# Optimization experiments

Hardware: AMD Instinct MI355X
Metric: run time of the kernel (lower is better)

## Reference

```python
import jax, jax.numpy as jnp
from jax import lax
import numpy as np


def _conv2d(x, w, b, pad):
    # x: NCHW, w: OIHW
    o = lax.conv_general_dilated(x, w, window_strides=(1, 1),
                                 padding=[(pad, pad), (pad, pad)],
                                 dimension_numbers=('NCHW', 'OIHW', 'NCHW'))
    return o + b[None, :, None, None]


def _maxpool(x, kh, kw):
    return lax.reduce_window(x, -jnp.inf, lax.max,
                             window_dimensions=(1, 1, kh, kw),
                             window_strides=(1, 1, kh, kw),
                             padding='VALID')


def _l2norm(x, axis):
    n = jnp.sqrt(jnp.sum(x * x, axis=axis, keepdims=True))
    return x / jnp.maximum(n, 1e-12)


def setup_inputs() -> dict:
    key = jax.random.key(0)
    ks = jax.random.split(key, 12)
    d = {}
    d['x'] = jax.random.normal(ks[0], (16, 128, 40, 200), dtype=jnp.float32)
    d['cluster_centers'] = jax.random.uniform(ks[1], (64, 128), dtype=jnp.float32)
    d['conv_w'] = jax.random.normal(ks[2], (64, 128, 1, 1), dtype=jnp.float32) * 0.05
    d['conv_b'] = jax.random.normal(ks[3], (64,), dtype=jnp.float32) * 0.05
    d['w1'] = jax.random.normal(ks[4], (256, 128, 5, 5), dtype=jnp.float32) * 0.02
    d['b1'] = jax.random.normal(ks[5], (256,), dtype=jnp.float32) * 0.02
    d['w2'] = jax.random.normal(ks[6], (512, 256, 5, 5), dtype=jnp.float32) * 0.02
    d['b2'] = jax.random.normal(ks[7], (512,), dtype=jnp.float32) * 0.02
    d['w3'] = jax.random.normal(ks[8], (1024, 512, 5, 5), dtype=jnp.float32) * 0.02
    d['b3'] = jax.random.normal(ks[9], (1024,), dtype=jnp.float32) * 0.02
    d['mlp_w'] = jax.random.normal(ks[10], (256, 9216), dtype=jnp.float32) * 0.01
    d['mlp_b'] = jax.random.normal(ks[11], (256,), dtype=jnp.float32) * 0.01
    return d


def reference(x, cluster_centers, conv_w, conv_b, w1, b1, w2, b2, w3, b3, mlp_w, mlp_b):
    N, C, H, W = x.shape
    K = conv_w.shape[0]
    P = H * W

    # soft assignment: 1x1 conv -> softmax over cluster axis
    sa = _conv2d(x, conv_w, conv_b, 0).reshape(N, K, P)
    a = jax.nn.softmax(sa, axis=1)                      # [N, K, P]

    x_flat = x.reshape(N, C, P)
    # sum_p a[n,k,p] * (x[n,c,p] - centers[k,c])  -- algebraically equal to
    # the explicit NxKxCxP residual tensor, computed without materializing it.
    vlad = jnp.einsum('nkp,ncp->nkc', a, x_flat) \
           - a.sum(axis=-1)[:, :, None] * cluster_centers[None, :, :]
    vlad = _l2norm(vlad, axis=2)                        # intra-norm per cluster
    vlad = _l2norm(vlad.reshape(N, K * C), axis=1)      # [N, K*C]

    # CNN branch
    h = _conv2d(x, w1, b1, 2)
    h = jnp.where(h >= 0, h, 0.2 * h)                   # LeakyReLU(0.2)
    h = _maxpool(h, 2, 2)
    h = _conv2d(h, w2, b2, 2)
    h = jnp.where(h >= 0, h, 0.2 * h)
    h = _maxpool(h, 4, 4)
    h = _conv2d(h, w3, b3, 2)
    h = _maxpool(h, 5, 25)                              # -> [N, 1024, 1, 1]
    x_feat = _l2norm(h.reshape(N, -1), axis=1)          # [N, 1024]

    feat = jnp.concatenate([vlad, x_feat], axis=1)      # [N, 9216]
    out = feat @ mlp_w.T + mlp_b
    return _l2norm(out, axis=1)
```

## Files before the change

kernel.cpp:

```cpp
#include <hip/hip_runtime.h>
#include <math.h>

#define K_ 64
#define C_ 128
#define NB 16
#define P_ 8000

typedef float f32x4 __attribute__((ext_vector_type(4)));
typedef short s16x8 __attribute__((ext_vector_type(8)));

__device__ __forceinline__ short f2bf(float v) {
    unsigned u = __float_as_uint(v);
    u += 0x7FFFu + ((u >> 16) & 1u);
    return (short)(u >> 16);
}
__device__ __forceinline__ float bf2f(ushort u) { return __uint_as_float(((unsigned)u) << 16); }

__device__ __forceinline__ void stage16(const void* g, void* l) {
    __builtin_amdgcn_global_load_lds(
        (const __attribute__((address_space(1))) void*)g,
        (__attribute__((address_space(3))) void*)l, 16, 0, 0);
}

__global__ void k_transpose_tiled(const float* __restrict__ in, float* __restrict__ out,
                                  int Co, int E)
{
    __shared__ float t[32][33];
    const int e0  = blockIdx.x * 32;
    const int co0 = blockIdx.y * 32;
    for (int i = threadIdx.y; i < 32; i += 8) {
        int co = co0 + i, e = e0 + threadIdx.x;
        t[i][threadIdx.x] = (co < Co && e < E) ? in[(size_t)co * E + e] : 0.f;
    }
    __syncthreads();
    for (int i = threadIdx.y; i < 32; i += 8) {
        int e = e0 + i, co = co0 + threadIdx.x;
        if (e < E && co < Co) out[(size_t)e * Co + co] = t[threadIdx.x][i];
    }
}

__global__ void k_nchw_to_nhwc(const float* __restrict__ in, ushort* __restrict__ out,
                               int C, int P)
{
    __shared__ ushort t[32][33];
    const int n  = blockIdx.z;
    const int p0 = blockIdx.x * 32;
    const int c0 = blockIdx.y * 32;
    for (int i = threadIdx.y; i < 32; i += 8) {
        int c = c0 + i, p = p0 + threadIdx.x;
        t[i][threadIdx.x] = (c < C && p < P) ? (ushort)f2bf(in[((size_t)n * C + c) * P + p]) : 0;
    }
    __syncthreads();
    for (int i = threadIdx.y; i < 32; i += 8) {
        int p = p0 + i, c = c0 + threadIdx.x;
        if (p < P && c < C) out[((size_t)n * P + p) * C + c] = t[threadIdx.x][i];
    }
}

__global__ void k_wprep(const float* __restrict__ w, short* __restrict__ wb,
                        int Co, int Cin, int total)
{
    int idx = blockIdx.x * blockDim.x + threadIdx.x;
    if (idx >= total) return;
    int cl = idx & 31;
    int rest = idx >> 5;
    int co = rest % Co;
    int rest2 = rest / Co;
    int t = rest2 % 25;
    int ck = rest2 / 25;
    float v = w[((size_t)co * Cin + (ck << 5) + cl) * 25 + t];
    wb[idx] = f2bf(v);
}

template<int SR, int NC, int WR, int WC16, int IS3, int PL>
__global__ __launch_bounds__(256) void k_conv_mfma(
    const ushort* __restrict__ in, const s16x8* __restrict__ wb,
    const float* __restrict__ bias, ushort* __restrict__ outb, float* __restrict__ outf,
    const ushort* __restrict__ zg,
    int Cin, int Co, int H, int W, int WT, int leaky, int nck, int xpc, int PT)
{
    constexpr int NT   = 8;
    constexpr int TOT  = SR * NC * 4;
    constexpr int TOTP = (TOT + 63) & ~63;
    __shared__ s16x8 xin[TOTP];

    const int tid  = threadIdx.x;
    const int lane = tid & 63;
    const int wid  = tid >> 6;
    const int wm   = wid;
    const int n16  = lane & 15;
    const int g    = lane >> 4;

    const int lid  = blockIdx.x;
    const int xcd  = lid & 7;
    const int rrr  = lid >> 3;
    const int co_blk = xcd / xpc;
    const int posn = rrr * xpc + (xcd % xpc);
    const int n    = posn / PT;
    const int bx   = posn % PT;

    const int h0  = IS3 ? 0 : (bx / WT) * WR;
    const int w0  = IS3 ? 0 : (bx % WT) * (WC16 * 16);
    const int ks  = IS3 ? bx : 0;
    const int co0 = co_blk * 256;

    int ph[NT], pw[NT];
    if (IS3) {
        #pragma unroll
        for (int nt = 0; nt < NT; ++nt) {
            int pos = nt * 16 + n16;
            int h = pos / 25;
            int w = pos - h * 25;
            if (h > 4) { h = 0; w = 0; }
            ph[nt] = h; pw[nt] = w;
        }
    }

    f32x4 acc[4][NT];
    #pragma unroll
    for (int i = 0; i < 4; ++i)
        #pragma unroll
        for (int j = 0; j < NT; ++j) acc[i][j] = f32x4{0.f, 0.f, 0.f, 0.f};

    const int ck0 = IS3 ? ks * nck : 0;
    const int ckend = ck0 + nck;

    auto stage_input = [&](int ck) {
        for (int c = wid; c * 64 < TOTP; c += 4) {
            int u = c * 64 + lane;
            int row = u / (NC * 4);
            int rem = u - row * (NC * 4);
            int col = rem >> 2;
            int s   = rem & 3;
            int g8  = (s - (col >> 1) - row) & 3;
            int gh = h0 + row - 2, gw = w0 + col - 2;
            const void* src =
                (u < TOT && (unsigned)gh < (unsigned)H && (unsigned)gw < (unsigned)W)
                ? (const void*)(in + ((size_t)(n * H + gh) * W + gw) * Cin + (ck << 5) + (g8 << 3))
                : (const void*)zg;
            stage16(src, (void*)&xin[c * 64]);
        }
    };

    for (int ck = ck0; ck < ckend; ++ck) {
        if (ck != ck0) __syncthreads();
        stage_input(ck);
        __syncthreads();

        const s16x8* wbc = wb + ((size_t)(ck * 25) * Co + co0 + wm * 64 + n16) * 4 + g;

        s16x8 wreg[3][4];
        #pragma unroll
        for (int mt = 0; mt < 4; ++mt) wreg[0][mt] = wbc[mt * 64];
        #pragma unroll
        for (int mt = 0; mt < 4; ++mt) wreg[1][mt] = wbc[(size_t)Co * 4 + mt * 64];

        #pragma unroll
        for (int t = 0; t < 25; ++t) {
            if (t < 23) {
                const s16x8* wn = wbc + (size_t)(t + 2) * Co * 4;
                #pragma unroll
                for (int mt = 0; mt < 4; ++mt) wreg[(t + 2) % 3][mt] = wn[mt * 64];
            }
            const int r = t / 5, s = t - (t / 5) * 5;

            s16x8 bf[NT];
            #pragma unroll
            for (int nt = 0; nt < NT; ++nt) {
                int row, col;
                if (IS3) { row = ph[nt] + r; col = pw[nt] + s; }
                else {
                    int rr = nt / WC16, cc = nt - rr * WC16;
                    row = rr + r;
                    col = cc * 16 + n16 + s;
                }
                bf[nt] = xin[(row * NC + col) * 4 + ((g + (col >> 1) + row) & 3)];
            }
            __builtin_amdgcn_s_setprio(1);
            #pragma unroll
            for (int mt = 0; mt < 4; ++mt)
                #pragma unroll
                for (int nt = 0; nt < NT; ++nt)
                    acc[mt][nt] = __builtin_amdgcn_mfma_f32_16x16x32_bf16(
                        wreg[t % 3][mt], bf[nt], acc[mt][nt], 0, 0, 0);
            __builtin_amdgcn_s_setprio(0);
        }
    }

    if constexpr (IS3) {
        #pragma unroll
        for (int mt = 0; mt < 4; ++mt) {
            #pragma unroll
            for (int reg = 0; reg < 4; ++reg) {
                const int co = co0 + wm * 64 + mt * 16 + g * 4 + reg;
                #pragma unroll
                for (int nt = 0; nt < NT; ++nt) {
                    int pos = nt * 16 + n16;
                    if (pos < 125)
                        outf[((size_t)(ks * NB + n) * Co + co) * 125 + pos] = acc[mt][nt][reg];
                }
            }
        }
    } else if constexpr (PL == 2) {
        const int Hout = H >> 1, Wout = W >> 1;
        #pragma unroll
        for (int mt = 0; mt < 4; ++mt) {
            const int cb = co0 + wm * 64 + mt * 16 + g * 4;
            #pragma unroll
            for (int pr = 0; pr < 2; ++pr) {
                #pragma unroll
                for (int cc = 0; cc < 2; ++cc) {
                    ushort4 pkd;
                    #pragma unroll
                    for (int reg = 0; reg < 4; ++reg) {
                        float a0 = acc[mt][(2 * pr) * 2 + cc][reg] + bias[cb + reg];
                        float a1 = acc[mt][(2 * pr + 1) * 2 + cc][reg] + bias[cb + reg];
                        a0 = (a0 >= 0.f) ? a0 : 0.2f * a0;
                        a1 = (a1 >= 0.f) ? a1 : 0.2f * a1;
                        float m = fmaxf(a0, a1);
                        m = fmaxf(m, __shfl_xor(m, 1));
                        ((ushort*)&pkd)[reg] = (ushort)f2bf(m);
                    }
                    if ((n16 & 1) == 0) {
                        int ho = (h0 >> 1) + pr;
                        int wo = (w0 >> 1) + cc * 8 + (n16 >> 1);
                        if (wo < Wout)
                            *(ushort4*)(outb + ((size_t)(n * Hout + ho) * Wout + wo) * Co + cb) = pkd;
                    }
                }
            }
        }
    } else if constexpr (PL == 4) {
        const int Hout = H >> 2, Wout = W >> 2;
        #pragma unroll
        for (int mt = 0; mt < 4; ++mt) {
            const int cb = co0 + wm * 64 + mt * 16 + g * 4;
            #pragma unroll
            for (int cc = 0; cc < 2; ++cc) {
                ushort4 pkd;
                #pragma unroll
                for (int reg = 0; reg < 4; ++reg) {
                    float m = -INFINITY;
                    #pragma unroll
                    for (int rr = 0; rr < 4; ++rr) {
                        float a = acc[mt][rr * 2 + cc][reg] + bias[cb + reg];
                        a = (a >= 0.f) ? a : 0.2f * a;
                        m = fmaxf(m, a);
                    }
                    m = fmaxf(m, __shfl_xor(m, 1));
                    m = fmaxf(m, __shfl_xor(m, 2));
                    ((ushort*)&pkd)[reg] = (ushort)f2bf(m);
                }
                if ((n16 & 3) == 0) {
                    int ho = h0 >> 2;
                    int wo = (w0 >> 2) + cc * 4 + (n16 >> 2);
                    if (wo < Wout)
                        *(ushort4*)(outb + ((size_t)(n * Hout + ho) * Wout + wo) * Co + cb) = pkd;
                }
            }
        }
    } else {
        #pragma unroll
        for (int mt = 0; mt < 4; ++mt) {
            const int cobase = co0 + wm * 64 + mt * 16 + g * 4;
            const float b0 = bias[cobase + 0];
            const float b1 = bias[cobase + 1];
            const float b2 = bias[cobase + 2];
            const float b3 = bias[cobase + 3];
            #pragma unroll
            for (int nt = 0; nt < NT; ++nt) {
                int rr = nt / WC16, cc = nt - rr * WC16;
                int h  = h0 + rr;
                int wp = w0 + cc * 16 + n16;
                if (h < H && wp < W) {
                    float v0 = acc[mt][nt][0] + b0;
                    float v1 = acc[mt][nt][1] + b1;
                    float v2 = acc[mt][nt][2] + b2;
                    float v3 = acc[mt][nt][3] + b3;
                    if (leaky) {
                        v0 = (v0 >= 0.f) ? v0 : 0.2f * v0;
                        v1 = (v1 >= 0.f) ? v1 : 0.2f * v1;
                        v2 = (v2 >= 0.f) ? v2 : 0.2f * v2;
                        v3 = (v3 >= 0.f) ? v3 : 0.2f * v3;
                    }
                    ushort4 pkd;
                    pkd.x = (ushort)f2bf(v0);
                    pkd.y = (ushort)f2bf(v1);
                    pkd.z = (ushort)f2bf(v2);
                    pkd.w = (ushort)f2bf(v3);
                    *(ushort4*)(outb + ((size_t)(n * H + h) * W + wp) * Co + cobase) = pkd;
                }
            }
        }
    }
}

__global__ __launch_bounds__(256) void k_vlad_partial(
    const float* __restrict__ x,
    const float* __restrict__ convw_t,
    const float* __restrict__ convb,
    float* __restrict__ pv,
    float* __restrict__ pa)
{
    __shared__ float xs[C_][64];
    __shared__ float als[64][K_];
    __shared__ float pgsum[4][K_];

    const int tid = threadIdx.x;
    const int chunk = blockIdx.x;
    const int n = blockIdx.y;
    const int p0 = chunk * 64;

    const float* xn = x + (size_t)n * C_ * P_ + p0;
    for (int i = tid; i < C_ * 64; i += 256) {
        int c = i >> 6, pp = i & 63;
        xs[c][pp] = xn[(size_t)c * P_ + pp];
    }
    __syncthreads();

    const int k  = tid & 63;
    const int pg = tid >> 6;

    float sa[16];
    const float bk = convb[k];
    #pragma unroll
    for (int j = 0; j < 16; ++j) sa[j] = bk;
    for (int c = 0; c < C_; ++c) {
        float wv = convw_t[c * K_ + k];
        const float4* xp = (const float4*)&xs[c][pg * 16];
        #pragma unroll
        for (int q = 0; q < 4; ++q) {
            float4 xv = xp[q];
            sa[q*4+0] += wv * xv.x;
            sa[q*4+1] += wv * xv.y;
            sa[q*4+2] += wv * xv.z;
            sa[q*4+3] += wv * xv.w;
        }
    }

    float asum_loc = 0.f;
    #pragma unroll
    for (int j = 0; j < 16; ++j) {
        float m = sa[j];
        for (int d = 32; d >= 1; d >>= 1) m = fmaxf(m, __shfl_xor(m, d));
        float e = __expf(sa[j] - m);
        float s = e;
        for (int d = 32; d >= 1; d >>= 1) s += __shfl_xor(s, d);
        float a = e / s;
        als[pg * 16 + j][k] = a;
        asum_loc += a;
    }
    pgsum[pg][k] = asum_loc;
    __syncthreads();
    if (tid < K_) {
        pa[((size_t)n * 125 + chunk) * K_ + tid] =
            pgsum[0][tid] + pgsum[1][tid] + pgsum[2][tid] + pgsum[3][tid];
    }

    const int q = pg;
    float acc[32];
    #pragma unroll
    for (int j = 0; j < 32; ++j) acc[j] = 0.f;
    for (int p = 0; p < 64; p += 4) {
        float a0 = als[p+0][k], a1 = als[p+1][k], a2 = als[p+2][k], a3 = als[p+3][k];
        #pragma unroll
        for (int j = 0; j < 32; ++j) {
            const float4 xv = *(const float4*)&xs[q*32 + j][p];
            acc[j] += a0*xv.x + a1*xv.y + a2*xv.z + a3*xv.w;
        }
    }
    float* pvp = pv + ((((size_t)n * 125 + chunk) * K_ + k) * C_ + q * 32);
    #pragma unroll
    for (int j = 0; j < 32; ++j) pvp[j] = acc[j];
}

__global__ void k_vlad_reduce(const float* __restrict__ pv, float* __restrict__ vlad_raw)
{
    int idx = blockIdx.x * blockDim.x + threadIdx.x;
    if (idx >= NB * 8192) return;
    int n = idx >> 13;
    int rest = idx & 8191;
    const float* p = pv + (size_t)n * 125 * 8192 + rest;
    float s = 0.f;
    for (int ch = 0; ch < 125; ++ch) s += p[(size_t)ch * 8192];
    vlad_raw[(size_t)n * 8192 + rest] = s;
}

__global__ void k_asum_reduce(const float* __restrict__ pa, float* __restrict__ asum)
{
    int idx = blockIdx.x * blockDim.x + threadIdx.x;
    if (idx >= NB * K_) return;
    const float* p = pa + (size_t)(idx >> 6) * 125 * K_ + (idx & 63);
    float s = 0.f;
    for (int ch = 0; ch < 125; ++ch) s += p[ch * K_];
    asum[idx] = s;
}

__global__ __launch_bounds__(128) void k_vlad_finalize(
    const float* __restrict__ vlad_raw, const float* __restrict__ asum,
    const float* __restrict__ centers, float* __restrict__ feat)
{
    __shared__ float red[2];
    const int k = blockIdx.x, n = blockIdx.y, c = threadIdx.x;
    float v = vlad_raw[((size_t)n * K_ + k) * C_ + c] - asum[n * K_ + k] * centers[k * C_ + c];
    float ss = v * v;
    for (int d = 32; d >= 1; d >>= 1) ss += __shfl_xor(ss, d);
    if ((threadIdx.x & 63) == 0) red[threadIdx.x >> 6] = ss;
    __syncthreads();
    float denom = fmaxf(sqrtf(red[0] + red[1]), 1e-12f);
    feat[(size_t)n * 9216 + k * C_ + c] = v / denom;
}

__global__ void k_pool3_feat(const float* __restrict__ part, const float* __restrict__ bias,
                             float* __restrict__ feat)
{
    int idx = blockIdx.x * blockDim.x + threadIdx.x;
    if (idx >= NB * 1024) return;
    int n = idx >> 10, c = idx & 1023;
    const size_t kstride = (size_t)NB * 1024 * 125;
    const float* p = part + ((size_t)n * 1024 + c) * 125;
    const float b = bias[c];
    float m = -INFINITY;
    for (int i = 0; i < 125; ++i) {
        float s = 0.f;
        #pragma unroll
        for (int ksl = 0; ksl < 8; ++ksl) s += p[i + ksl * kstride];
        m = fmaxf(m, b + s);
    }
    feat[(size_t)n * 9216 + 8192 + c] = m;
}

__global__ __launch_bounds__(256) void k_featnorm(const float* __restrict__ feat,
                                                  float* __restrict__ scale)
{
    __shared__ float r1s[4], r2s[4];
    const int n = blockIdx.x;
    const int tid = threadIdx.x;
    const int wid = tid >> 6;
    float s1 = 0.f, s2 = 0.f;
    const float* f = feat + (size_t)n * 9216;
    for (int i = tid; i < 9216; i += 256) {
        float v = f[i];
        if (i < 8192) s1 += v * v; else s2 += v * v;
    }
    for (int d = 32; d >= 1; d >>= 1) { s1 += __shfl_xor(s1, d); s2 += __shfl_xor(s2, d); }
    if ((tid & 63) == 0) { r1s[wid] = s1; r2s[wid] = s2; }
    __syncthreads();
    if (tid == 0) {
        scale[n * 2 + 0] = 1.f / fmaxf(sqrtf(r1s[0] + r1s[1] + r1s[2] + r1s[3]), 1e-12f);
        scale[n * 2 + 1] = 1.f / fmaxf(sqrtf(r2s[0] + r2s[1] + r2s[2] + r2s[3]), 1e-12f);
    }
}

__global__ __launch_bounds__(256) void k_mlp_part(
    const float* __restrict__ feat, const float* __restrict__ scale,
    const float* __restrict__ wt,
    float* __restrict__ part)
{
    __shared__ float fs[576];
    const int n  = blockIdx.x >> 4;
    const int sl = blockIdx.x & 15;
    const int tid = threadIdx.x;
    const int base = sl * 576;
    for (int j = tid; j < 576; j += 256) {
        int idx = base + j;
        fs[j] = feat[(size_t)n * 9216 + idx] * scale[n * 2 + (idx < 8192 ? 0 : 1)];
    }
    __syncthreads();
    float a0 = 0.f, a1 = 0.f;
    for (int j = 0; j < 576; j += 2) {
        a0 += fs[j]     * wt[(size_t)(base + j)     * 256 + tid];
        a1 += fs[j + 1] * wt[(size_t)(base + j + 1) * 256 + tid];
    }
    part[((size_t)n * 16 + sl) * 256 + tid] = a0 + a1;
}

__global__ __launch_bounds__(256) void k_mlp_final(
    const float* __restrict__ part, const float* __restrict__ bias,
    float* __restrict__ outp)
{
    __shared__ float red[4];
    const int n = blockIdx.x;
    const int tid = threadIdx.x;
    float a = bias[tid];
    #pragma unroll
    for (int s = 0; s < 16; ++s) a += part[((size_t)n * 16 + s) * 256 + tid];
    float ss = a * a;
    for (int d = 32; d >= 1; d >>= 1) ss += __shfl_xor(ss, d);
    if ((tid & 63) == 0) red[tid >> 6] = ss;
    __syncthreads();
    const float inv = 1.f / fmaxf(sqrtf(red[0] + red[1] + red[2] + red[3]), 1e-12f);
    outp[n * 256 + tid] = a * inv;
}

extern "C" void kernel_launch(void* const* d_in, const int* in_sizes, int n_in,
                              void* d_out, int out_size, void* d_ws, size_t ws_size,
                              hipStream_t stream)
{
    const float* x      = (const float*)d_in[0];
    const float* cents  = (const float*)d_in[1];
    const float* conv_w = (const float*)d_in[2];
    const float* conv_b = (const float*)d_in[3];
    const float* w1     = (const float*)d_in[4];
    const float* b1     = (const float*)d_in[5];
    const float* w2     = (const float*)d_in[6];
    const float* b2     = (const float*)d_in[7];
    const float* w3     = (const float*)d_in[8];
    const float* b3     = (const float*)d_in[9];
    const float* mlp_w  = (const float*)d_in[10];
    const float* mlp_b  = (const float*)d_in[11];
    float* outp = (float*)d_out;

    char* ws = (char*)d_ws;
    size_t off = 0;
    auto alloc = [&](size_t bytes) -> void* {
        off = (off + 255) & ~(size_t)255;
        void* p = ws + off;
        off += bytes;
        return p;
    };
    ushort* zguard  = (ushort*)alloc(256);
    float*  convw_t = (float*)alloc((size_t)64 * 128 * 4);
    float*  mwt     = (float*)alloc((size_t)9216 * 256 * 4);
    short*  wb1     = (short*)alloc((size_t)819200 * 2);
    short*  wb2     = (short*)alloc((size_t)3276800 * 2);
    short*  wb3     = (short*)alloc((size_t)13107200 * 2);
    ushort* x_cl    = (ushort*)alloc((size_t)NB * 8000 * 128 * 2);
    float*  vlad_raw= (float*)alloc((size_t)NB * 8192 * 4);
    float*  asum    = (float*)alloc((size_t)NB * K_ * 4);
    float*  feat    = (float*)alloc((size_t)NB * 9216 * 4);
    float*  pa      = (float*)alloc((size_t)NB * 125 * K_ * 4);
    float*  scale   = (float*)alloc((size_t)NB * 2 * 4);
    float*  mpart   = (float*)alloc((size_t)NB * 16 * 256 * 4);
    ushort* pool2b  = (ushort*)alloc((size_t)NB * 125 * 512 * 2);
    char*   slabA   = (char*)alloc((size_t)8 * NB * 1024 * 125 * 4);
    ushort* slabB   = (ushort*)alloc((size_t)NB * 2000 * 256 * 2);

    hipMemsetAsync(zguard, 0, 256, stream);

    {
        dim3 blk(32, 8);
        k_transpose_tiled<<<dim3(4, 2), blk, 0, stream>>>(conv_w, convw_t, 64, 128);
        k_transpose_tiled<<<dim3(288, 8), blk, 0, stream>>>(mlp_w, mwt, 256, 9216);
        k_wprep<<<(819200 + 255) / 256, 256, 0, stream>>>(w1, wb1, 256, 128, 819200);
        k_wprep<<<(3276800 + 255) / 256, 256, 0, stream>>>(w2, wb2, 512, 256, 3276800);
        k_wprep<<<(13107200 + 255) / 256, 256, 0, stream>>>(w3, wb3, 1024, 512, 13107200);
        k_nchw_to_nhwc<<<dim3(250, 4, NB), blk, 0, stream>>>(x, x_cl, 128, 8000);
    }

    k_vlad_partial<<<dim3(125, NB), 256, 0, stream>>>(x, convw_t, conv_b, (float*)slabA, pa);
    k_vlad_reduce<<<(NB * 8192 + 255) / 256, 256, 0, stream>>>((float*)slabA, vlad_raw);
    k_asum_reduce<<<(NB * K_ + 255) / 256, 256, 0, stream>>>(pa, asum);
    k_vlad_finalize<<<dim3(K_, NB), 128, 0, stream>>>(vlad_raw, asum, cents, feat);

    k_conv_mfma<8, 36, 4, 2, 0, 2><<<1120, 256, 0, stream>>>(
        x_cl, (const s16x8*)wb1, b1, slabB, nullptr, zguard,
        128, 256, 40, 200, 7, 1, 4, 8, 70);
    k_conv_mfma<8, 36, 4, 2, 0, 4><<<640, 256, 0, stream>>>(
        slabB, (const s16x8*)wb2, b2, pool2b, nullptr, zguard,
        256, 512, 20, 100, 4, 1, 8, 4, 20);
    k_conv_mfma<9, 29, 4, 2, 1, 1><<<512, 256, 0, stream>>>(
        pool2b, (const s16x8*)wb3, b3, nullptr, (float*)slabA, zguard,
        512, 1024, 5, 25, 1, 0, 2, 2, 8);
    k_pool3_feat<<<(NB * 1024 + 255) / 256, 256, 0, stream>>>((float*)slabA, b3, feat);

    k_featnorm<<<NB, 256, 0, stream>>>(feat, scale);
    k_mlp_part<<<NB * 16, 256, 0, stream>>>(feat, scale, mwt, mpart);
    k_mlp_final<<<NB, 256, 0, stream>>>(mpart, mlp_b, outp);
}
```

Measured before the change: 1.002 ms.

## Accumulate VLAD partials over four chunks per block and fuse reductions into finalize

Each k_vlad_partial block now loops over up to four 64-pixel chunks, keeping its residual accumulator in registers. This cuts the partial-sum buffer from 125 to 32 slices per image. The separate vlad and asum reduce kernels are removed, and the finalize kernel sums the 32 slices directly, which cuts partial-buffer traffic and two launches. The cost is a much smaller grid for the partial kernel (512 blocks instead of 2000), so it gets less parallelism and latency hiding.

```diff
diff --git a/kernel.cpp b/kernel.cpp
--- a/kernel.cpp
+++ b/kernel.cpp
@@ -5,6 +5,7 @@
 #define C_ 128
 #define NB 16
 #define P_ 8000
+#define VG 32
 
 typedef float f32x4 __attribute__((ext_vector_type(4)));
 typedef short s16x8 __attribute__((ext_vector_type(8)));
@@ -307,102 +308,93 @@
     __shared__ float pgsum[4][K_];
 
     const int tid = threadIdx.x;
-    const int chunk = blockIdx.x;
-    const int n = blockIdx.y;
-    const int p0 = chunk * 64;
-
-    const float* xn = x + (size_t)n * C_ * P_ + p0;
-    for (int i = tid; i < C_ * 64; i += 256) {
-        int c = i >> 6, pp = i & 63;
-        xs[c][pp] = xn[(size_t)c * P_ + pp];
-    }
-    __syncthreads();
-
-    const int k  = tid & 63;
-    const int pg = tid >> 6;
-
-    float sa[16];
-    const float bk = convb[k];
-    #pragma unroll
-    for (int j = 0; j < 16; ++j) sa[j] = bk;
-    for (int c = 0; c < C_; ++c) {
-        float wv = convw_t[c * K_ + k];
-        const float4* xp = (const float4*)&xs[c][pg * 16];
-        #pragma unroll
-        for (int q = 0; q < 4; ++q) {
-            float4 xv = xp[q];
-            sa[q*4+0] += wv * xv.x;
-            sa[q*4+1] += wv * xv.y;
-            sa[q*4+2] += wv * xv.z;
-            sa[q*4+3] += wv * xv.w;
-        }
-    }
-
-    float asum_loc = 0.f;
-    #pragma unroll
-    for (int j = 0; j < 16; ++j) {
-        float m = sa[j];
-        for (int d = 32; d >= 1; d >>= 1) m = fmaxf(m, __shfl_xor(m, d));
-        float e = __expf(sa[j] - m);
-        float s = e;
-        for (int d = 32; d >= 1; d >>= 1) s += __shfl_xor(s, d);
-        float a = e / s;
-        als[pg * 16 + j][k] = a;
-        asum_loc += a;
-    }
-    pgsum[pg][k] = asum_loc;
-    __syncthreads();
-    if (tid < K_) {
-        pa[((size_t)n * 125 + chunk) * K_ + tid] =
-            pgsum[0][tid] + pgsum[1][tid] + pgsum[2][tid] + pgsum[3][tid];
-    }
-
-    const int q = pg;
+    const int grp = blockIdx.x;
+    const int n   = blockIdx.y;
+    const int k   = tid & 63;
+    const int pg  = tid >> 6;
+    const int q   = pg;
+
+    const int cB = grp * 4;
+    const int cE = (cB + 4 < 125) ? (cB + 4) : 125;
+
     float acc[32];
     #pragma unroll
     for (int j = 0; j < 32; ++j) acc[j] = 0.f;
-    for (int p = 0; p < 64; p += 4) {
-        float a0 = als[p+0][k], a1 = als[p+1][k], a2 = als[p+2][k], a3 = als[p+3][k];
-        #pragma unroll
-        for (int j = 0; j < 32; ++j) {
-            const float4 xv = *(const float4*)&xs[q*32 + j][p];
-            acc[j] += a0*xv.x + a1*xv.y + a2*xv.z + a3*xv.w;
-        }
-    }
-    float* pvp = pv + ((((size_t)n * 125 + chunk) * K_ + k) * C_ + q * 32);
+    float pa_acc = 0.f;
+    const float bk = convb[k];
+
+    for (int chunk = cB; chunk < cE; ++chunk) {
+        if (chunk != cB) __syncthreads();
+        const int p0 = chunk * 64;
+        const float* xn = x + (size_t)n * C_ * P_ + p0;
+        for (int i = tid; i < C_ * 64; i += 256) {
+            int c = i >> 6, pp = i & 63;
+            xs[c][pp] = xn[(size_t)c * P_ + pp];
+        }
+        __syncthreads();
+
+        float sa[16];
+        #pragma unroll
+        for (int j = 0; j < 16; ++j) sa[j] = bk;
+        for (int c = 0; c < C_; ++c) {
+            float wv = convw_t[c * K_ + k];
+            const float4* xp = (const float4*)&xs[c][pg * 16];
+            #pragma unroll
+            for (int q2 = 0; q2 < 4; ++q2) {
+                float4 xv = xp[q2];
+                sa[q2*4+0] += wv * xv.x;
+                sa[q2*4+1] += wv * xv.y;
+                sa[q2*4+2] += wv * xv.z;
+                sa[q2*4+3] += wv * xv.w;
+            }
+        }
+
+        float asum_loc = 0.f;
+        #pragma unroll
+        for (int j = 0; j < 16; ++j) {
+            float m = sa[j];
+            for (int d = 32; d >= 1; d >>= 1) m = fmaxf(m, __shfl_xor(m, d));
+            float e = __expf(sa[j] - m);
+            float s = e;
+            for (int d = 32; d >= 1; d >>= 1) s += __shfl_xor(s, d);
+            float a = e / s;
+            als[pg * 16 + j][k] = a;
+            asum_loc += a;
+        }
+        pgsum[pg][k] = asum_loc;
+        __syncthreads();
+        if (tid < K_)
+            pa_acc += pgsum[0][tid] + pgsum[1][tid] + pgsum[2][tid] + pgsum[3][tid];
+
+        for (int p = 0; p < 64; p += 4) {
+            float a0 = als[p+0][k], a1 = als[p+1][k], a2 = als[p+2][k], a3 = als[p+3][k];
+            #pragma unroll
+            for (int j = 0; j < 32; ++j) {
+                const float4 xv = *(const float4*)&xs[q*32 + j][p];
+                acc[j] += a0*xv.x + a1*xv.y + a2*xv.z + a3*xv.w;
+            }
+        }
+    }
+
+    float* pvp = pv + ((((size_t)n * VG + grp) * K_ + k) * C_ + q * 32);
     #pragma unroll
     for (int j = 0; j < 32; ++j) pvp[j] = acc[j];
-}
-
-__global__ void k_vlad_reduce(const float* __restrict__ pv, float* __restrict__ vlad_raw)
-{
-    int idx = blockIdx.x * blockDim.x + threadIdx.x;
-    if (idx >= NB * 8192) return;
-    int n = idx >> 13;
-    int rest = idx & 8191;
-    const float* p = pv + (size_t)n * 125 * 8192 + rest;
-    float s = 0.f;
-    for (int ch = 0; ch < 125; ++ch) s += p[(size_t)ch * 8192];
-    vlad_raw[(size_t)n * 8192 + rest] = s;
-}
-
-__global__ void k_asum_reduce(const float* __restrict__ pa, float* __restrict__ asum)
-{
-    int idx = blockIdx.x * blockDim.x + threadIdx.x;
-    if (idx >= NB * K_) return;
-    const float* p = pa + (size_t)(idx >> 6) * 125 * K_ + (idx & 63);
-    float s = 0.f;
-    for (int ch = 0; ch < 125; ++ch) s += p[ch * K_];
-    asum[idx] = s;
-}
-
-__global__ __launch_bounds__(128) void k_vlad_finalize(
-    const float* __restrict__ vlad_raw, const float* __restrict__ asum,
+    if (tid < K_) pa[((size_t)n * VG + grp) * K_ + tid] = pa_acc;
+}
+
+__global__ __launch_bounds__(128) void k_vlad_fin(
+    const float* __restrict__ pv, const float* __restrict__ pa,
     const float* __restrict__ centers, float* __restrict__ feat)
 {
     __shared__ float red[2];
     const int k = blockIdx.x, n = blockIdx.y, c = threadIdx.x;
-    float v = vlad_raw[((size_t)n * K_ + k) * C_ + c] - asum[n * K_ + k] * centers[k * C_ + c];
+    float s = 0.f;
+    for (int g2 = 0; g2 < VG; ++g2)
+        s += pv[(((size_t)n * VG + g2) * K_ + k) * C_ + c];
+    float at = 0.f;
+    for (int g2 = 0; g2 < VG; ++g2)
+        at += pa[((size_t)n * VG + g2) * K_ + k];
+    float v = s - at * centers[k * C_ + c];
     float ss = v * v;
     for (int d = 32; d >= 1; d >>= 1) ss += __shfl_xor(ss, d);
     if ((threadIdx.x & 63) == 0) red[threadIdx.x >> 6] = ss;
@@ -526,10 +518,9 @@
     short*  wb2     = (short*)alloc((size_t)3276800 * 2);
     short*  wb3     = (short*)alloc((size_t)13107200 * 2);
     ushort* x_cl    = (ushort*)alloc((size_t)NB * 8000 * 128 * 2);
-    float*  vlad_raw= (float*)alloc((size_t)NB * 8192 * 4);
-    float*  asum    = (float*)alloc((size_t)NB * K_ * 4);
+    float*  pvbuf   = (float*)alloc((size_t)NB * VG * K_ * C_ * 4);
+    float*  pabuf   = (float*)alloc((size_t)NB * VG * K_ * 4);
     float*  feat    = (float*)alloc((size_t)NB * 9216 * 4);
-    float*  pa      = (float*)alloc((size_t)NB * 125 * K_ * 4);
     float*  scale   = (float*)alloc((size_t)NB * 2 * 4);
     float*  mpart   = (float*)alloc((size_t)NB * 16 * 256 * 4);
     ushort* pool2b  = (ushort*)alloc((size_t)NB * 125 * 512 * 2);
@@ -548,10 +539,8 @@
         k_nchw_to_nhwc<<<dim3(250, 4, NB), blk, 0, stream>>>(x, x_cl, 128, 8000);
     }
 
-    k_vlad_partial<<<dim3(125, NB), 256, 0, stream>>>(x, convw_t, conv_b, (float*)slabA, pa);
-    k_vlad_reduce<<<(NB * 8192 + 255) / 256, 256, 0, stream>>>((float*)slabA, vlad_raw);
-    k_asum_reduce<<<(NB * K_ + 255) / 256, 256, 0, stream>>>(pa, asum);
-    k_vlad_finalize<<<dim3(K_, NB), 128, 0, stream>>>(vlad_raw, asum, cents, feat);
+    k_vlad_partial<<<dim3(VG, NB), 256, 0, stream>>>(x, convw_t, conv_b, pvbuf, pabuf);
+    k_vlad_fin<<<dim3(K_, NB), 128, 0, stream>>>(pvbuf, pabuf, cents, feat);
 
     k_conv_mfma<8, 36, 4, 2, 0, 2><<<1120, 256, 0, stream>>>(
         x_cl, (const s16x8*)wb1, b1, slabB, nullptr, zguard,
```

New measurement: 995.0 us. Within noise of the previous version (-0.7%).
